# Performance work log

Hardware: AMD Instinct MI355X
Metric: run time of the kernel (lower is better)

## Reference

```python
import jax, jax.numpy as jnp
import numpy as np

B = 4096
NP = 196  # 14x14 patches


def setup_inputs() -> dict:
    key = jax.random.key(0)
    k1, k2, k3 = jax.random.split(key, 3)
    x = jax.random.uniform(k1, (B, 1, 28, 28), dtype=jnp.float32)
    params = jax.random.normal(k2, (8,), dtype=jnp.float32)      # [rz0, ry0, rz1, ry1, ...]
    W = jax.random.normal(k3, (10, 784), dtype=jnp.float32) * 0.03
    b = jnp.zeros((10,), dtype=jnp.float32)
    return {"x": x, "params": params, "W": W, "b": b}


def reference(x, params, W, b):
    bsz = x.shape[0]
    # Extract 2x2 patches: per-patch qubit order [x[r,c], x[r,c+1], x[r+1,c], x[r+1,c+1]]
    d = x.reshape(bsz, 14, 2, 14, 2).transpose(0, 1, 3, 2, 4).reshape(bsz, NP, 4)
    alpha = params[0::2]  # rz angles, per wire [4]
    beta = params[1::2]   # ry angles, per wire [4]
    # Per-wire single-qubit chain on |0>: Ry(beta) Rz(alpha) Ry(d) Ry(d) |0>
    # Ry(2d)|0> = [cos d, sin d]; then Rz phases; then Ry(beta) rotation.
    cb = jnp.cos(0.5 * beta)
    sb = jnp.sin(0.5 * beta)
    pm = jnp.exp(-0.5j * alpha)  # e^{-i a/2}
    pp = jnp.exp(0.5j * alpha)   # e^{+i a/2}
    a = pm * jnp.cos(d)          # [B,P,4] complex64
    c = pp * jnp.sin(d)
    u = jnp.stack([cb * a - sb * c, sb * a + cb * c], axis=-1)  # [B,P,4,2]
    # Product state over 4 wires -> [B,P,2,2,2,2]
    st = jnp.einsum('bpi,bpj,bpk,bpl->bpijkl',
                    u[:, :, 0], u[:, :, 1], u[:, :, 2], u[:, :, 3])
    # CNOT(0,1): flip target axis (j) where control axis (i) == 1
    st = jnp.concatenate([st[:, :, 0:1], st[:, :, 1:2, ::-1]], axis=2)
    # CNOT(2,3): flip target axis (l) where control axis (k) == 1
    st = jnp.concatenate([st[:, :, :, :, 0:1, :], st[:, :, :, :, 1:2, ::-1]], axis=4)
    probs = (st * jnp.conj(st)).real  # [B,P,2,2,2,2]
    z = jnp.array([1.0, -1.0], dtype=jnp.float32)
    e0 = jnp.einsum('bpijkl,i->bp', probs, z)
    e1 = jnp.einsum('bpijkl,j->bp', probs, z)
    e2 = jnp.einsum('bpijkl,k->bp', probs, z)
    e3 = jnp.einsum('bpijkl,l->bp', probs, z)
    feats = jnp.stack([e0, e1, e2, e3], axis=-1).reshape(bsz, NP * 4)  # patch-major, matches torch.cat
    logits = feats @ W.T + b
    return jax.nn.log_softmax(logits, axis=-1)
```

## Files before the change

kernel.cpp:

```cpp
#include <hip/hip_runtime.h>
#include <math.h>


__global__ __launch_bounds__(256) void quanv_kernel(
    const float* __restrict__ x,
    const float* __restrict__ params,
    const float* __restrict__ W,
    const float* __restrict__ bias,
    float* __restrict__ out)
{
    const int t = threadIdx.x;
    const int wave = t >> 6;
    const int lane = t & 63;
    const int b = blockIdx.x * 4 + wave;

    float A[4], Bc[4];
#pragma unroll
    for (int k = 0; k < 4; k++) {
        const float al = params[2 * k];
        const float be = params[2 * k + 1];
        A[k]  = __cosf(be);
        Bc[k] = __sinf(be) * __cosf(al);
    }

    const float* img = x + (size_t)b * 784;
    const float4* W4 = (const float4*)W;

    float lg[10];
#pragma unroll
    for (int c = 0; c < 10; c++) lg[c] = 0.0f;

#pragma unroll
    for (int k = 0; k < 4; k++) {
        const int praw = lane + 64 * k;
        const bool valid = (praw < 196);
        const int p = valid ? praw : 195;
        const int i = p / 14;
        const int j = p - 14 * i;

        const float2 d01 = *(const float2*)(img + i * 56 + 2 * j);
        const float2 d23 = *(const float2*)(img + i * 56 + 28 + 2 * j);

        const float E0 = A[0] * __cosf(2.0f * d01.x) - Bc[0] * __sinf(2.0f * d01.x);
        const float E1 = A[1] * __cosf(2.0f * d01.y) - Bc[1] * __sinf(2.0f * d01.y);
        const float E2 = A[2] * __cosf(2.0f * d23.x) - Bc[2] * __sinf(2.0f * d23.x);
        const float E3 = A[3] * __cosf(2.0f * d23.y) - Bc[3] * __sinf(2.0f * d23.y);

        float f0 = E0;
        float f1 = E0 * E1;
        float f2 = E2;
        float f3 = E2 * E3;
        if (!valid) { f0 = 0.0f; f1 = 0.0f; f2 = 0.0f; f3 = 0.0f; }

#pragma unroll
        for (int c = 0; c < 10; c++) {
            const float4 w = W4[c * 196 + p];
            lg[c] += f0 * w.x + f1 * w.y + f2 * w.z + f3 * w.w;
        }
    }

#pragma unroll
    for (int c = 0; c < 10; c++) {
        float v = lg[c];
#pragma unroll
        for (int off = 32; off > 0; off >>= 1) v += __shfl_down(v, off, 64);
        lg[c] = v;
    }

    if (lane == 0) {
        float mx = -1e30f;
#pragma unroll
        for (int c = 0; c < 10; c++) {
            lg[c] += bias[c];
            mx = fmaxf(mx, lg[c]);
        }
        float sum = 0.0f;
#pragma unroll
        for (int c = 0; c < 10; c++) sum += __expf(lg[c] - mx);
        const float lse = mx + __logf(sum);
        float* ob = out + (size_t)b * 10;
#pragma unroll
        for (int c = 0; c < 10; c++) ob[c] = lg[c] - lse;
    }
}

extern "C" void kernel_launch(void* const* d_in, const int* in_sizes, int n_in,
                              void* d_out, int out_size, void* d_ws, size_t ws_size,
                              hipStream_t stream) {
    const float* x      = (const float*)d_in[0];
    const float* params = (const float*)d_in[1];
    const float* W      = (const float*)d_in[2];
    const float* bias   = (const float*)d_in[3];
    float* out          = (float*)d_out;

    quanv_kernel<<<1024, 256, 0, stream>>>(x, params, W, bias, out);
}
```

Baseline: 70.91 us.

## Split each image across two waves and combine partial logits in shared memory

```diff
diff --git a/kernel.cpp b/kernel.cpp
--- a/kernel.cpp
+++ b/kernel.cpp
@@ -2,7 +2,7 @@
 #include <math.h>
 
 
-__global__ __launch_bounds__(256) void quanv_kernel(
+__global__ __launch_bounds__(256, 8) void quanv_kernel(
     const float* __restrict__ x,
     const float* __restrict__ params,
     const float* __restrict__ W,
@@ -12,7 +12,9 @@
     const int t = threadIdx.x;
     const int wave = t >> 6;
     const int lane = t & 63;
-    const int b = blockIdx.x * 4 + wave;
+    const int img_in_blk = wave >> 1;
+    const int half = wave & 1;
+    const int b = blockIdx.x * 2 + img_in_blk;
 
     float A[4], Bc[4];
 #pragma unroll
@@ -31,10 +33,10 @@
     for (int c = 0; c < 10; c++) lg[c] = 0.0f;
 
 #pragma unroll
-    for (int k = 0; k < 4; k++) {
-        const int praw = lane + 64 * k;
-        const bool valid = (praw < 196);
-        const int p = valid ? praw : 195;
+    for (int k = 0; k < 2; k++) {
+        const int off = 64 * k + lane;
+        const bool valid = (off < 98);
+        const int p = half * 98 + (valid ? off : 97);
         const int i = p / 14;
         const int j = p - 14 * i;
 
@@ -46,14 +48,18 @@
         const float E2 = A[2] * __cosf(2.0f * d23.x) - Bc[2] * __sinf(2.0f * d23.x);
         const float E3 = A[3] * __cosf(2.0f * d23.y) - Bc[3] * __sinf(2.0f * d23.y);
 
-        float f0 = E0;
-        float f1 = E0 * E1;
-        float f2 = E2;
-        float f3 = E2 * E3;
-        if (!valid) { f0 = 0.0f; f1 = 0.0f; f2 = 0.0f; f3 = 0.0f; }
+        const float f0 = valid ? E0 : 0.0f;
+        const float f1 = f0 * E1;
+        const float f2 = valid ? E2 : 0.0f;
+        const float f3 = f2 * E3;
 
 #pragma unroll
-        for (int c = 0; c < 10; c++) {
+        for (int c = 0; c < 5; c++) {
+            const float4 w = W4[c * 196 + p];
+            lg[c] += f0 * w.x + f1 * w.y + f2 * w.z + f3 * w.w;
+        }
+#pragma unroll
+        for (int c = 5; c < 10; c++) {
             const float4 w = W4[c * 196 + p];
             lg[c] += f0 * w.x + f1 * w.y + f2 * w.z + f3 * w.w;
         }
@@ -63,24 +69,32 @@
     for (int c = 0; c < 10; c++) {
         float v = lg[c];
 #pragma unroll
-        for (int off = 32; off > 0; off >>= 1) v += __shfl_down(v, off, 64);
+        for (int o = 32; o > 0; o >>= 1) v += __shfl_down(v, o, 64);
         lg[c] = v;
     }
 
+    __shared__ float ls[4][10];
     if (lane == 0) {
+#pragma unroll
+        for (int c = 0; c < 10; c++) ls[wave][c] = lg[c];
+    }
+    __syncthreads();
+
+    if (t < 2) {
+        float l[10];
         float mx = -1e30f;
 #pragma unroll
         for (int c = 0; c < 10; c++) {
-            lg[c] += bias[c];
-            mx = fmaxf(mx, lg[c]);
+            l[c] = ls[2 * t][c] + ls[2 * t + 1][c] + bias[c];
+            mx = fmaxf(mx, l[c]);
         }
         float sum = 0.0f;
 #pragma unroll
-        for (int c = 0; c < 10; c++) sum += __expf(lg[c] - mx);
+        for (int c = 0; c < 10; c++) sum += __expf(l[c] - mx);
         const float lse = mx + __logf(sum);
-        float* ob = out + (size_t)b * 10;
+        float* ob = out + ((size_t)blockIdx.x * 2 + t) * 10;
 #pragma unroll
-        for (int c = 0; c < 10; c++) ob[c] = lg[c] - lse;
+        for (int c = 0; c < 10; c++) ob[c] = l[c] - lse;
     }
 }
 
@@ -93,5 +107,5 @@
     const float* bias   = (const float*)d_in[3];
     float* out          = (float*)d_out;
 
-    quanv_kernel<<<1024, 256, 0, stream>>>(x, params, W, bias, out);
+    quanv_kernel<<<2048, 256, 0, stream>>>(x, params, W, bias, out);
 }
```

Result: no change. 71.95 us (+1.5%).
